# Performance work log

Hardware: AMD Instinct MI355X
Metric: run time of the kernel (lower is better)

Reference implementation:

```python
import jax, jax.numpy as jnp
import numpy as np

NOOBJ_LAMBDA = 0.5
COORD_LAMBDA = 5.0


def _cxcywh_to_xyxy(b):
    cx, cy, w, h = b[..., 0], b[..., 1], b[..., 2], b[..., 3]
    return jnp.stack([cx - w / 2, cy - h / 2, cx + w / 2, cy + h / 2], axis=-1)


def _pairwise_iou(a, b):
    # a: [B, N, 4] xyxy (preds), b: [B, M, 4] xyxy (targets) -> [B, N, M]
    lt = jnp.maximum(a[:, :, None, :2], b[:, None, :, :2])
    rb = jnp.minimum(a[:, :, None, 2:], b[:, None, :, 2:])
    wh = jnp.clip(rb - lt, 0.0)
    inter = wh[..., 0] * wh[..., 1]
    area_a = (a[..., 2] - a[..., 0]) * (a[..., 3] - a[..., 1])
    area_b = (b[..., 2] - b[..., 0]) * (b[..., 3] - b[..., 1])
    union = area_a[:, :, None] + area_b[:, None, :] - inter
    return inter / jnp.where(union > 0, union, 1.0)


def setup_inputs() -> dict:
    key = jax.random.key(0)
    kp, kt, km = jax.random.split(key, 3)
    B = 8192
    # positive values so sqrt(w), sqrt(h) is well-defined (as the torch code assumes)
    pred = jax.random.uniform(kp, (B, 7, 7, 30), dtype=jnp.float32, minval=0.05, maxval=1.0)
    target = jax.random.uniform(kt, (B, 7, 7, 30), dtype=jnp.float32, minval=0.05, maxval=1.0)
    # target confidence channel (index 4) is the obj/noobj indicator: 0 or 1
    obj = (jax.random.uniform(km, (B, 7, 7)) < 0.2).astype(jnp.float32)
    target = target.at[..., 4].set(obj)
    return {"pred_tensor": pred, "target_tensor": target}


def reference(pred_tensor, target_tensor):
    B = pred_tensor.shape[0]
    pred = pred_tensor.reshape(B, 49, 30)
    target = target_tensor.reshape(B, 49, 30)

    conf_t = target[..., 4]            # [B,49]
    noobj = conf_t == 0                # [B,49]
    obj = conf_t > 0                   # [B,49]

    # --- no-object confidence loss (channels 4 and 9) ---
    d4 = pred[..., 4] - target[..., 4]
    d9 = pred[..., 9] - target[..., 9]
    noobj_loss = jnp.sum(jnp.where(noobj, d4 * d4 + d9 * d9, 0.0))

    # --- object cells: 2 boxes per cell, padded to all 49 cells with a mask ---
    pb = pred[..., :10].reshape(B, 98, 5)
    tb = target[..., :10].reshape(B, 98, 5)
    box_mask = jnp.repeat(obj, 2, axis=1)  # [B,98]

    p_xyxy = _cxcywh_to_xyxy(pb[..., :4])
    t_xyxy = _cxcywh_to_xyxy(tb[..., :4])
    iou = _pairwise_iou(p_xyxy, t_xyxy)  # [B,98,98]
    pair_mask = box_mask[:, :, None] & box_mask[:, None, :]
    iou = jnp.where(pair_mask, iou, 0.0)
    max_iou = jnp.max(iou, axis=1)       # max over pred boxes, per target box [B,98]
    cmask = (max_iou != 0) & box_mask    # [B,98]

    cm = cmask.astype(pred.dtype)
    # coord (cx,cy) loss
    dxy = pb[..., :2] - tb[..., :2]
    coord_loss_cxcy = jnp.sum(cm * jnp.sum(dxy * dxy, axis=-1))
    # coord (sqrt w, sqrt h) loss
    dwh = jnp.sqrt(pb[..., 2:4]) - jnp.sqrt(tb[..., 2:4])
    coord_loss_wh = jnp.sum(cm * jnp.sum(dwh * dwh, axis=-1))
    # object confidence loss
    dconf = pb[..., 4] - tb[..., 4]
    obj_loss = jnp.sum(cm * dconf * dconf)

    # --- class loss over object cells ---
    dcls = pred[..., 10:] - target[..., 10:]
    cls_loss = jnp.sum(obj.astype(pred.dtype) * jnp.sum(dcls * dcls, axis=-1))

    bsz = jnp.asarray(B, pred.dtype)
    batch_cls_loss = cls_loss / bsz
    batch_obj_loss = (obj_loss + noobj_loss * NOOBJ_LAMBDA) / bsz
    batch_coord_loss = (coord_loss_cxcy + coord_loss_wh) * COORD_LAMBDA / bsz
    batch_loss = batch_cls_loss + batch_obj_loss + batch_coord_loss
    return (batch_loss, batch_cls_loss, batch_obj_loss, batch_coord_loss)
```

## Files before the change

### kernel.cpp

```cpp
#include <hip/hip_runtime.h>

#define CH 30
#define CELLS 49
#define ROWF 1470
#define WPB 4

__device__ __forceinline__ float waveReduce(float v) {
    #pragma unroll
    for (int o = 32; o > 0; o >>= 1) v += __shfl_xor(v, o, 64);
    return v;
}

__global__ __launch_bounds__(256) void yolo_main(const float* __restrict__ pred,
                                                 const float* __restrict__ targ,
                                                 float* __restrict__ ws, int B,
                                                 int NB) {
    const int w = threadIdx.x >> 6;
    const int lane = threadIdx.x & 63;
    const int r = blockIdx.x * WPB + w;

    __shared__ float4 boxS[WPB][2 * CELLS];
    __shared__ int clist[WPB][CELLS];
    __shared__ float sred[WPB][3];

    float cls = 0.f, objc = 0.f, coord = 0.f;

    if (r < B) {
        const float* P = pred + (size_t)r * ROWF;
        const float* T = targ + (size_t)r * ROWF;

        const int cl = lane < CELLS ? lane : CELLS - 1;
        const float t4 = T[cl * CH + 4];
        const float p4 = P[cl * CH + 4];
        const float t9 = T[cl * CH + 9];
        const float p9 = P[cl * CH + 9];

        const bool act = lane < CELLS;
        const bool isObj = act && (t4 > 0.f);
        const unsigned long long m = __ballot(isObj);

        if (act && !isObj) {
            const float d4 = p4 - t4, d9 = p9 - t9;
            objc += 0.5f * (d4 * d4 + d9 * d9);
        }

        const int nObj = __popcll(m);
        if (isObj) clist[w][__popcll(m & ((1ull << lane) - 1ull))] = lane;

        if (nObj) {
            const int nCls = nObj * 20;
            for (int base = 0; base < nCls; base += 64) {
                const int idx = base + lane;
                if (idx < nCls) {
                    const int cc = (idx * 3277) >> 16;
                    const int ch = 10 + (idx - cc * 20);
                    const int c = clist[w][cc];
                    const float dv = P[c * CH + ch] - T[c * CH + ch];
                    cls += dv * dv;
                }
            }

            const int nBox = 2 * nObj;
            for (int e = lane; e < nBox; e += 64) {
                const int c = clist[w][e >> 1];
                const float* pb = P + c * CH + (e & 1) * 5;
                const float cx = pb[0], cy = pb[1], bw = pb[2], bh = pb[3];
                boxS[w][e] = make_float4(cx - 0.5f * bw, cy - 0.5f * bh,
                                         cx + 0.5f * bw, cy + 0.5f * bh);
            }

            for (int e = lane; e < nBox; e += 64) {
                const int c = clist[w][e >> 1];
                const float* tb = T + c * CH + (e & 1) * 5;
                const float tcx = tb[0], tcy = tb[1], tw = tb[2], th = tb[3];
                const float tx1 = tcx - 0.5f * tw, ty1 = tcy - 0.5f * th;
                const float tx2 = tcx + 0.5f * tw, ty2 = tcy + 0.5f * th;
                const float ta = (tx2 - tx1) * (ty2 - ty1);
                float maxiou = 0.f;
                for (int i = 0; i < nBox; ++i) {
                    const float4 pb4 = boxS[w][i];
                    const float lx = fmaxf(pb4.x, tx1), ly = fmaxf(pb4.y, ty1);
                    const float rx = fminf(pb4.z, tx2), ry = fminf(pb4.w, ty2);
                    const float iw = fmaxf(rx - lx, 0.f), ih = fmaxf(ry - ly, 0.f);
                    const float inter = iw * ih;
                    const float pa = (pb4.z - pb4.x) * (pb4.w - pb4.y);
                    const float un = pa + ta - inter;
                    const float iou = inter / (un > 0.f ? un : 1.f);
                    maxiou = fmaxf(maxiou, iou);
                }
                if (maxiou != 0.f) {
                    const float* pb = P + c * CH + (e & 1) * 5;
                    const float dcx = pb[0] - tcx, dcy = pb[1] - tcy;
                    coord += dcx * dcx + dcy * dcy;
                    const float dw = sqrtf(pb[2]) - sqrtf(tw);
                    const float dh = sqrtf(pb[3]) - sqrtf(th);
                    coord += dw * dw + dh * dh;
                    const float dc = pb[4] - tb[4];
                    objc += dc * dc;
                }
            }
        }
    }

    cls = waveReduce(cls); objc = waveReduce(objc); coord = waveReduce(coord);
    if (lane == 0) { sred[w][0] = cls; sred[w][1] = objc; sred[w][2] = coord; }
    __syncthreads();
    if (threadIdx.x == 0) {
        float C = 0.f, O = 0.f, X = 0.f;
        #pragma unroll
        for (int k = 0; k < WPB; ++k) { C += sred[k][0]; O += sred[k][1]; X += sred[k][2]; }
        ws[blockIdx.x] = C;
        ws[NB + blockIdx.x] = O;
        ws[2 * NB + blockIdx.x] = X;
    }
}

__global__ __launch_bounds__(1024) void yolo_reduce(const float* __restrict__ ws,
                                                    float* __restrict__ out,
                                                    int NB, float invB) {
    const int tid = threadIdx.x;
    const int w = tid >> 6, lane = tid & 63;
    float c = 0.f, o = 0.f, x = 0.f;
    for (int i = tid; i < NB; i += 1024) {
        c += ws[i];
        o += ws[NB + i];
        x += ws[2 * NB + i];
    }
    c = waveReduce(c); o = waveReduce(o); x = waveReduce(x);
    __shared__ float sred[16][3];
    if (lane == 0) { sred[w][0] = c; sred[w][1] = o; sred[w][2] = x; }
    __syncthreads();
    if (tid == 0) {
        float C = 0.f, O = 0.f, X = 0.f;
        #pragma unroll
        for (int k = 0; k < 16; ++k) { C += sred[k][0]; O += sred[k][1]; X += sred[k][2]; }
        const float bcls = C * invB;
        const float bobj = O * invB;
        const float bcoord = X * 5.0f * invB;
        out[0] = bcls + bobj + bcoord;
        out[1] = bcls;
        out[2] = bobj;
        out[3] = bcoord;
    }
}

extern "C" void kernel_launch(void* const* d_in, const int* in_sizes, int n_in,
                              void* d_out, int out_size, void* d_ws, size_t ws_size,
                              hipStream_t stream) {
    const float* pred = (const float*)d_in[0];
    const float* targ = (const float*)d_in[1];
    float* ws = (float*)d_ws;
    float* out = (float*)d_out;
    const int B = in_sizes[0] / ROWF;
    const int NB = (B + WPB - 1) / WPB;

    yolo_main<<<NB, 256, 0, stream>>>(pred, targ, ws, B, NB);
    yolo_reduce<<<1, 1024, 0, stream>>>(ws, out, NB, 1.0f / (float)B);
}
```

Measured before the change: 126.2 us.

## Stage two rows per wave into LDS with direct global-to-LDS loads

Each wave now handles two consecutive batch rows and copies both pred and target rows in full into shared memory using global_load_lds 16-byte transfers, replacing scattered per-element global reads. Class and no-object losses are then computed from LDS in a dense, coalesced sweep over all channels, weighted by the object mask, while the IoU matching reads boxes from LDS. Blocks shrink to 128 threads, and each wave uses about 23KB of LDS, which may limit occupancy. The sweep also reads every class channel, including those of non-object cells.

```diff
diff --git a/kernel.cpp b/kernel.cpp
--- a/kernel.cpp
+++ b/kernel.cpp
@@ -3,7 +3,11 @@
 #define CH 30
 #define CELLS 49
 #define ROWF 1470
-#define WPB 4
+#define REGF 2940
+#define WPB 2
+#define RPBLK 4
+#define FULLI 11
+#define TAILL 31
 
 __device__ __forceinline__ float waveReduce(float v) {
     #pragma unroll
@@ -11,55 +15,148 @@
     return v;
 }
 
-__global__ __launch_bounds__(256) void yolo_main(const float* __restrict__ pred,
+__global__ __launch_bounds__(128) void yolo_main(const float* __restrict__ pred,
                                                  const float* __restrict__ targ,
                                                  float* __restrict__ ws, int B,
                                                  int NB) {
     const int w = threadIdx.x >> 6;
     const int lane = threadIdx.x & 63;
-    const int r = blockIdx.x * WPB + w;
-
+    const int r0 = (blockIdx.x * WPB + w) * 2;
+
+    __shared__ float stage[WPB][2][REGF];
     __shared__ float4 boxS[WPB][2 * CELLS];
     __shared__ int clist[WPB][CELLS];
     __shared__ float sred[WPB][3];
 
     float cls = 0.f, objc = 0.f, coord = 0.f;
 
-    if (r < B) {
-        const float* P = pred + (size_t)r * ROWF;
-        const float* T = targ + (size_t)r * ROWF;
-
-        const int cl = lane < CELLS ? lane : CELLS - 1;
-        const float t4 = T[cl * CH + 4];
-        const float p4 = P[cl * CH + 4];
-        const float t9 = T[cl * CH + 9];
-        const float p9 = P[cl * CH + 9];
-
+    if (r0 < B && (B - r0) >= 2) {
+        const float* P = pred + (size_t)r0 * ROWF;
+        const float* T = targ + (size_t)r0 * ROWF;
+        float* lP = &stage[w][0][0];
+        float* lT = &stage[w][1][0];
+
+        #pragma unroll
+        for (int k = 0; k < FULLI; ++k) {
+            __builtin_amdgcn_global_load_lds(
+                (const __attribute__((address_space(1))) float*)(P + k * 256 + lane * 4),
+                (__attribute__((address_space(3))) float*)(lP + k * 256), 16, 0, 0);
+            __builtin_amdgcn_global_load_lds(
+                (const __attribute__((address_space(1))) float*)(T + k * 256 + lane * 4),
+                (__attribute__((address_space(3))) float*)(lT + k * 256), 16, 0, 0);
+        }
+        if (lane < TAILL) {
+            __builtin_amdgcn_global_load_lds(
+                (const __attribute__((address_space(1))) float*)(P + FULLI * 256 + lane * 4),
+                (__attribute__((address_space(3))) float*)(lP + FULLI * 256), 16, 0, 0);
+            __builtin_amdgcn_global_load_lds(
+                (const __attribute__((address_space(1))) float*)(T + FULLI * 256 + lane * 4),
+                (__attribute__((address_space(3))) float*)(lT + FULLI * 256), 16, 0, 0);
+        }
+
+        asm volatile("s_waitcnt vmcnt(0)" ::: "memory");
+
+        const int cc = lane < CELLS ? lane : CELLS - 1;
+        unsigned long long m[2];
+        m[0] = __ballot((lane < CELLS) && (lT[cc * CH + 4] > 0.f));
+        m[1] = __ballot((lane < CELLS) && (lT[ROWF + cc * CH + 4] > 0.f));
+
+        #pragma unroll
+        for (int k = 0; k < 23; ++k) {
+            const int q = lane + k * 64;
+            if (q < 2 * 735) {
+                const int row = q >= 735;
+                const int pr = q - row * 735;
+                const int cell = (pr * 17477) >> 18;
+                const int ch0 = 2 * (pr - cell * 15);
+                const float wobj = (float)((m[row] >> cell) & 1ull);
+                const float2 pq = *(const float2*)(lP + 2 * q);
+                const float2 tq = *(const float2*)(lT + 2 * q);
+                const float dx = pq.x - tq.x, dy = pq.y - tq.y;
+                cls += (ch0 >= 10) ? wobj * (dx * dx + dy * dy) : 0.f;
+                const float nn = (ch0 == 4 ? dx * dx : 0.f)
+                               + (ch0 == 8 ? dy * dy : 0.f);
+                objc += 0.5f * (1.f - wobj) * nn;
+            }
+        }
+
+        for (int row = 0; row < 2; ++row) {
+            const unsigned long long mask = m[row];
+            const int nBox = 2 * __popcll(mask);
+            if (!nBox) continue;
+            const float* Pr = lP + row * ROWF;
+            const float* Tr = lT + row * ROWF;
+            const bool isObj = (lane < CELLS) && ((mask >> lane) & 1ull);
+            if (isObj) clist[w][__popcll(mask & ((1ull << lane) - 1ull))] = lane;
+
+            for (int e = lane; e < nBox; e += 64) {
+                const int c = clist[w][e >> 1];
+                const float* pb = Pr + c * CH + (e & 1) * 5;
+                const float cx = pb[0], cy = pb[1], bw = pb[2], bh = pb[3];
+                boxS[w][e] = make_float4(cx - 0.5f * bw, cy - 0.5f * bh,
+                                         cx + 0.5f * bw, cy + 0.5f * bh);
+            }
+
+            for (int e = lane; e < nBox; e += 64) {
+                const int c = clist[w][e >> 1];
+                const float* tb = Tr + c * CH + (e & 1) * 5;
+                const float tcx = tb[0], tcy = tb[1], tw = tb[2], th = tb[3];
+                const float tx1 = tcx - 0.5f * tw, ty1 = tcy - 0.5f * th;
+                const float tx2 = tcx + 0.5f * tw, ty2 = tcy + 0.5f * th;
+                const float ta = (tx2 - tx1) * (ty2 - ty1);
+                float maxiou = 0.f;
+                for (int i = 0; i < nBox; ++i) {
+                    const float4 pb4 = boxS[w][i];
+                    const float lx = fmaxf(pb4.x, tx1), ly = fmaxf(pb4.y, ty1);
+                    const float rx = fminf(pb4.z, tx2), ry = fminf(pb4.w, ty2);
+                    const float iw = fmaxf(rx - lx, 0.f), ih = fmaxf(ry - ly, 0.f);
+                    const float inter = iw * ih;
+                    const float pa = (pb4.z - pb4.x) * (pb4.w - pb4.y);
+                    const float un = pa + ta - inter;
+                    const float iou = inter / (un > 0.f ? un : 1.f);
+                    maxiou = fmaxf(maxiou, iou);
+                }
+                if (maxiou != 0.f) {
+                    const float* pb = Pr + c * CH + (e & 1) * 5;
+                    const float dcx = pb[0] - tcx, dcy = pb[1] - tcy;
+                    coord += dcx * dcx + dcy * dcy;
+                    const float dw = sqrtf(pb[2]) - sqrtf(tw);
+                    const float dh = sqrtf(pb[3]) - sqrtf(th);
+                    coord += dw * dw + dh * dh;
+                    const float dc = pb[4] - tb[4];
+                    objc += dc * dc;
+                }
+            }
+        }
+    } else if (r0 < B) {
+        const float* P = pred + (size_t)r0 * ROWF;
+        const float* T = targ + (size_t)r0 * ROWF;
+        const int cc = lane < CELLS ? lane : CELLS - 1;
+        const float t4 = T[cc * CH + 4];
+        const float p4 = P[cc * CH + 4];
+        const float t9 = T[cc * CH + 9];
+        const float p9 = P[cc * CH + 9];
         const bool act = lane < CELLS;
         const bool isObj = act && (t4 > 0.f);
-        const unsigned long long m = __ballot(isObj);
-
+        const unsigned long long mask = __ballot(isObj);
         if (act && !isObj) {
             const float d4 = p4 - t4, d9 = p9 - t9;
             objc += 0.5f * (d4 * d4 + d9 * d9);
         }
-
-        const int nObj = __popcll(m);
-        if (isObj) clist[w][__popcll(m & ((1ull << lane) - 1ull))] = lane;
-
+        const int nObj = __popcll(mask);
+        if (isObj) clist[w][__popcll(mask & ((1ull << lane) - 1ull))] = lane;
         if (nObj) {
             const int nCls = nObj * 20;
             for (int base = 0; base < nCls; base += 64) {
                 const int idx = base + lane;
                 if (idx < nCls) {
-                    const int cc = (idx * 3277) >> 16;
-                    const int ch = 10 + (idx - cc * 20);
-                    const int c = clist[w][cc];
+                    const int ccc = (idx * 3277) >> 16;
+                    const int ch = 10 + (idx - ccc * 20);
+                    const int c = clist[w][ccc];
                     const float dv = P[c * CH + ch] - T[c * CH + ch];
                     cls += dv * dv;
                 }
             }
-
             const int nBox = 2 * nObj;
             for (int e = lane; e < nBox; e += 64) {
                 const int c = clist[w][e >> 1];
@@ -68,7 +165,6 @@
                 boxS[w][e] = make_float4(cx - 0.5f * bw, cy - 0.5f * bh,
                                          cx + 0.5f * bw, cy + 0.5f * bh);
             }
-
             for (int e = lane; e < nBox; e += 64) {
                 const int c = clist[w][e >> 1];
                 const float* tb = T + c * CH + (e & 1) * 5;
@@ -152,8 +248,8 @@
     float* ws = (float*)d_ws;
     float* out = (float*)d_out;
     const int B = in_sizes[0] / ROWF;
-    const int NB = (B + WPB - 1) / WPB;
-
-    yolo_main<<<NB, 256, 0, stream>>>(pred, targ, ws, B, NB);
+    const int NB = (B + RPBLK - 1) / RPBLK;
+
+    yolo_main<<<NB, 128, 0, stream>>>(pred, targ, ws, B, NB);
     yolo_reduce<<<1, 1024, 0, stream>>>(ws, out, NB, 1.0f / (float)B);
 }
```

Result: slower. 132.7 us (+5.1%).

## Stream rows into LDS with double-buffered async global_load_lds in persistent waves

Applied to the files above, without the earlier changes.

Converts the kernel to a persistent grid (768 blocks of 2 waves), where each wave loops over rows and prefetches the next row's pred and target into LDS using async global-to-LDS loads, double-buffered and sequenced with explicit waitcnt. The class and no-object losses are now computed as a dense coalesced float2 sweep over the whole staged row with obj-mask weights, replacing scattered per-object gathers. The aim is to overlap memory latency with compute and keep the bandwidth-bound read fully coalesced. In exchange it relies on hand-tuned vmcnt counts and a fixed block count, and adds a large LDS footprint per block that may reduce occupancy.

```diff
diff --git a/kernel.cpp b/kernel.cpp
--- a/kernel.cpp
+++ b/kernel.cpp
@@ -3,7 +3,11 @@
 #define CH 30
 #define CELLS 49
 #define ROWF 1470
-#define WPB 4
+#define WPB 2
+#define NBLK 768
+#define FULLI 22
+#define TAILL 62
+#define BUFF 1472
 
 __device__ __forceinline__ float waveReduce(float v) {
     #pragma unroll
@@ -11,67 +15,97 @@
     return v;
 }
 
-__global__ __launch_bounds__(256) void yolo_main(const float* __restrict__ pred,
+__global__ __launch_bounds__(128) void yolo_main(const float* __restrict__ pred,
                                                  const float* __restrict__ targ,
                                                  float* __restrict__ ws, int B,
-                                                 int NB) {
+                                                 int NW) {
     const int w = threadIdx.x >> 6;
     const int lane = threadIdx.x & 63;
-    const int r = blockIdx.x * WPB + w;
+    const int wid = blockIdx.x * WPB + w;
 
+    __shared__ float stage[WPB][2][2][BUFF];
     __shared__ float4 boxS[WPB][2 * CELLS];
     __shared__ int clist[WPB][CELLS];
     __shared__ float sred[WPB][3];
 
     float cls = 0.f, objc = 0.f, coord = 0.f;
 
-    if (r < B) {
-        const float* P = pred + (size_t)r * ROWF;
-        const float* T = targ + (size_t)r * ROWF;
+    auto issueRow = [&](int row, int buf) {
+        const float* P = pred + (size_t)row * ROWF;
+        const float* T = targ + (size_t)row * ROWF;
+        float* lp = &stage[w][buf][0][0];
+        float* lt = &stage[w][buf][1][0];
+        #pragma unroll
+        for (int k = 0; k < FULLI; ++k) {
+            __builtin_amdgcn_global_load_lds(
+                (const __attribute__((address_space(1))) float*)(P + k * 64 + lane),
+                (__attribute__((address_space(3))) float*)(lp + k * 64), 4, 0, 0);
+            __builtin_amdgcn_global_load_lds(
+                (const __attribute__((address_space(1))) float*)(T + k * 64 + lane),
+                (__attribute__((address_space(3))) float*)(lt + k * 64), 4, 0, 0);
+        }
+        if (lane < TAILL) {
+            __builtin_amdgcn_global_load_lds(
+                (const __attribute__((address_space(1))) float*)(P + FULLI * 64 + lane),
+                (__attribute__((address_space(3))) float*)(lp + FULLI * 64), 4, 0, 0);
+            __builtin_amdgcn_global_load_lds(
+                (const __attribute__((address_space(1))) float*)(T + FULLI * 64 + lane),
+                (__attribute__((address_space(3))) float*)(lt + FULLI * 64), 4, 0, 0);
+        }
+    };
 
-        const int cl = lane < CELLS ? lane : CELLS - 1;
-        const float t4 = T[cl * CH + 4];
-        const float p4 = P[cl * CH + 4];
-        const float t9 = T[cl * CH + 9];
-        const float p9 = P[cl * CH + 9];
+    if (wid < B) issueRow(wid, 0);
 
-        const bool act = lane < CELLS;
-        const bool isObj = act && (t4 > 0.f);
-        const unsigned long long m = __ballot(isObj);
+    int it = 0;
+    for (int row = wid; row < B; row += NW, ++it) {
+        const int cur = it & 1;
+        const int nxt = row + NW;
 
-        if (act && !isObj) {
-            const float d4 = p4 - t4, d9 = p9 - t9;
-            objc += 0.5f * (d4 * d4 + d9 * d9);
+        asm volatile("s_waitcnt lgkmcnt(0)" ::: "memory");
+        if (nxt < B) {
+            issueRow(nxt, cur ^ 1);
+            asm volatile("s_waitcnt vmcnt(46)" ::: "memory");
+        } else {
+            asm volatile("s_waitcnt vmcnt(0)" ::: "memory");
         }
 
-        const int nObj = __popcll(m);
+        const float* lp = &stage[w][cur][0][0];
+        const float* lt = &stage[w][cur][1][0];
+
+        const int cc = lane < CELLS ? lane : CELLS - 1;
+        const bool isObj = (lane < CELLS) && (lt[cc * CH + 4] > 0.f);
+        const unsigned long long m = __ballot(isObj);
         if (isObj) clist[w][__popcll(m & ((1ull << lane) - 1ull))] = lane;
 
-        if (nObj) {
-            const int nCls = nObj * 20;
-            for (int base = 0; base < nCls; base += 64) {
-                const int idx = base + lane;
-                if (idx < nCls) {
-                    const int cc = (idx * 3277) >> 16;
-                    const int ch = 10 + (idx - cc * 20);
-                    const int c = clist[w][cc];
-                    const float dv = P[c * CH + ch] - T[c * CH + ch];
-                    cls += dv * dv;
-                }
+        #pragma unroll
+        for (int k = 0; k < 12; ++k) {
+            const int q = lane + k * 64;
+            if (q < 735) {
+                const int cell = (q * 17477) >> 18;
+                const int ch0 = 2 * (q - cell * 15);
+                const float wobj = (float)((m >> cell) & 1ull);
+                const float2 pq = *(const float2*)(lp + 2 * q);
+                const float2 tq = *(const float2*)(lt + 2 * q);
+                const float dx = pq.x - tq.x, dy = pq.y - tq.y;
+                cls += (ch0 >= 10) ? wobj * (dx * dx + dy * dy) : 0.f;
+                const float nn = (ch0 == 4 ? dx * dx : 0.f)
+                               + (ch0 == 8 ? dy * dy : 0.f);
+                objc += 0.5f * (1.f - wobj) * nn;
             }
+        }
 
-            const int nBox = 2 * nObj;
+        const int nBox = 2 * __popcll(m);
+        if (nBox) {
             for (int e = lane; e < nBox; e += 64) {
                 const int c = clist[w][e >> 1];
-                const float* pb = P + c * CH + (e & 1) * 5;
+                const float* pb = lp + c * CH + (e & 1) * 5;
                 const float cx = pb[0], cy = pb[1], bw = pb[2], bh = pb[3];
                 boxS[w][e] = make_float4(cx - 0.5f * bw, cy - 0.5f * bh,
                                          cx + 0.5f * bw, cy + 0.5f * bh);
             }
-
             for (int e = lane; e < nBox; e += 64) {
                 const int c = clist[w][e >> 1];
-                const float* tb = T + c * CH + (e & 1) * 5;
+                const float* tb = lt + c * CH + (e & 1) * 5;
                 const float tcx = tb[0], tcy = tb[1], tw = tb[2], th = tb[3];
                 const float tx1 = tcx - 0.5f * tw, ty1 = tcy - 0.5f * th;
                 const float tx2 = tcx + 0.5f * tw, ty2 = tcy + 0.5f * th;
@@ -89,7 +123,7 @@
                     maxiou = fmaxf(maxiou, iou);
                 }
                 if (maxiou != 0.f) {
-                    const float* pb = P + c * CH + (e & 1) * 5;
+                    const float* pb = lp + c * CH + (e & 1) * 5;
                     const float dcx = pb[0] - tcx, dcy = pb[1] - tcy;
                     coord += dcx * dcx + dcy * dcy;
                     const float dw = sqrtf(pb[2]) - sqrtf(tw);
@@ -110,8 +144,8 @@
         #pragma unroll
         for (int k = 0; k < WPB; ++k) { C += sred[k][0]; O += sred[k][1]; X += sred[k][2]; }
         ws[blockIdx.x] = C;
-        ws[NB + blockIdx.x] = O;
-        ws[2 * NB + blockIdx.x] = X;
+        ws[NBLK + blockIdx.x] = O;
+        ws[2 * NBLK + blockIdx.x] = X;
     }
 }
 
@@ -152,8 +186,8 @@
     float* ws = (float*)d_ws;
     float* out = (float*)d_out;
     const int B = in_sizes[0] / ROWF;
-    const int NB = (B + WPB - 1) / WPB;
+    const int NW = NBLK * WPB;
 
-    yolo_main<<<NB, 256, 0, stream>>>(pred, targ, ws, B, NB);
-    yolo_reduce<<<1, 1024, 0, stream>>>(ws, out, NB, 1.0f / (float)B);
+    yolo_main<<<NBLK, 128, 0, stream>>>(pred, targ, ws, B, NW);
+    yolo_reduce<<<1, 1024, 0, stream>>>(ws, out, NBLK, 1.0f / (float)B);
 }
```

New measurement: 129.7 us. +2.8%, slower.

## Stage full pred/target rows into LDS via direct global-to-LDS loads

Applied to the files above, without the earlier changes.

Each wave now copies its entire 1470-float pred and target rows into shared memory using coalesced global_load_lds instructions. Each lane then reads its own cell's 30 channels from LDS into registers, replacing the earlier scattered global gathers and the compacted cell-list indirection. Class loss and the IoU/coordinate work are computed per object cell by that cell's own lane. Blocks shrink to 2 waves because of the larger LDS footprint (about 24KB per block). That may limit occupancy, and lanes holding non-object cells sit idle during the per-cell work.

```diff
diff --git a/kernel.cpp b/kernel.cpp
--- a/kernel.cpp
+++ b/kernel.cpp
@@ -3,7 +3,9 @@
 #define CH 30
 #define CELLS 49
 #define ROWF 1470
-#define WPB 4
+#define WPB 2
+#define FULLI 22
+#define TAILL 62
 
 __device__ __forceinline__ float waveReduce(float v) {
     #pragma unroll
@@ -11,7 +13,7 @@
     return v;
 }
 
-__global__ __launch_bounds__(256) void yolo_main(const float* __restrict__ pred,
+__global__ __launch_bounds__(128) void yolo_main(const float* __restrict__ pred,
                                                  const float* __restrict__ targ,
                                                  float* __restrict__ ws, int B,
                                                  int NB) {
@@ -19,8 +21,8 @@
     const int lane = threadIdx.x & 63;
     const int r = blockIdx.x * WPB + w;
 
+    __shared__ float stage[WPB][2][ROWF];
     __shared__ float4 boxS[WPB][2 * CELLS];
-    __shared__ int clist[WPB][CELLS];
     __shared__ float sred[WPB][3];
 
     float cls = 0.f, objc = 0.f, coord = 0.f;
@@ -28,51 +30,78 @@
     if (r < B) {
         const float* P = pred + (size_t)r * ROWF;
         const float* T = targ + (size_t)r * ROWF;
+        float* lP = &stage[w][0][0];
+        float* lT = &stage[w][1][0];
 
-        const int cl = lane < CELLS ? lane : CELLS - 1;
-        const float t4 = T[cl * CH + 4];
-        const float p4 = P[cl * CH + 4];
-        const float t9 = T[cl * CH + 9];
-        const float p9 = P[cl * CH + 9];
+        #pragma unroll
+        for (int k = 0; k < FULLI; ++k) {
+            __builtin_amdgcn_global_load_lds(
+                (const __attribute__((address_space(1))) float*)(P + k * 64 + lane),
+                (__attribute__((address_space(3))) float*)(lP + k * 64), 4, 0, 0);
+            __builtin_amdgcn_global_load_lds(
+                (const __attribute__((address_space(1))) float*)(T + k * 64 + lane),
+                (__attribute__((address_space(3))) float*)(lT + k * 64), 4, 0, 0);
+        }
+        if (lane < TAILL) {
+            __builtin_amdgcn_global_load_lds(
+                (const __attribute__((address_space(1))) float*)(P + FULLI * 64 + lane),
+                (__attribute__((address_space(3))) float*)(lP + FULLI * 64), 4, 0, 0);
+            __builtin_amdgcn_global_load_lds(
+                (const __attribute__((address_space(1))) float*)(T + FULLI * 64 + lane),
+                (__attribute__((address_space(3))) float*)(lT + FULLI * 64), 4, 0, 0);
+        }
+        asm volatile("s_waitcnt vmcnt(0)" ::: "memory");
 
         const bool act = lane < CELLS;
-        const bool isObj = act && (t4 > 0.f);
+        const int c = act ? lane : CELLS - 1;
+        const float2* pc = (const float2*)(lP + c * CH);
+        const float2* tc = (const float2*)(lT + c * CH);
+
+        float2 pA[15], tA[15];
+        #pragma unroll
+        for (int j = 0; j < 15; ++j) { pA[j] = pc[j]; tA[j] = tc[j]; }
+
+        const bool isObj = act && (tA[2].x > 0.f);
         const unsigned long long m = __ballot(isObj);
+        const int nBox = 2 * __popcll(m);
 
         if (act && !isObj) {
-            const float d4 = p4 - t4, d9 = p9 - t9;
+            const float d4 = pA[2].x - tA[2].x;
+            const float d9 = pA[4].y - tA[4].y;
             objc += 0.5f * (d4 * d4 + d9 * d9);
         }
 
-        const int nObj = __popcll(m);
-        if (isObj) clist[w][__popcll(m & ((1ull << lane) - 1ull))] = lane;
+        if (isObj) {
+            #pragma unroll
+            for (int j = 5; j < 15; ++j) {
+                const float dx = pA[j].x - tA[j].x;
+                const float dy = pA[j].y - tA[j].y;
+                cls += dx * dx + dy * dy;
+            }
+            const int rank = __popcll(m & ((1ull << lane) - 1ull));
+            boxS[w][2 * rank] = make_float4(pA[0].x - 0.5f * pA[1].x,
+                                            pA[0].y - 0.5f * pA[1].y,
+                                            pA[0].x + 0.5f * pA[1].x,
+                                            pA[0].y + 0.5f * pA[1].y);
+            boxS[w][2 * rank + 1] = make_float4(pA[2].y - 0.5f * pA[3].y,
+                                                pA[3].x - 0.5f * pA[4].x,
+                                                pA[2].y + 0.5f * pA[3].y,
+                                                pA[3].x + 0.5f * pA[4].x);
+        }
 
-        if (nObj) {
-            const int nCls = nObj * 20;
-            for (int base = 0; base < nCls; base += 64) {
-                const int idx = base + lane;
-                if (idx < nCls) {
-                    const int cc = (idx * 3277) >> 16;
-                    const int ch = 10 + (idx - cc * 20);
-                    const int c = clist[w][cc];
-                    const float dv = P[c * CH + ch] - T[c * CH + ch];
-                    cls += dv * dv;
-                }
-            }
-
-            const int nBox = 2 * nObj;
-            for (int e = lane; e < nBox; e += 64) {
-                const int c = clist[w][e >> 1];
-                const float* pb = P + c * CH + (e & 1) * 5;
-                const float cx = pb[0], cy = pb[1], bw = pb[2], bh = pb[3];
-                boxS[w][e] = make_float4(cx - 0.5f * bw, cy - 0.5f * bh,
-                                         cx + 0.5f * bw, cy + 0.5f * bh);
-            }
-
-            for (int e = lane; e < nBox; e += 64) {
-                const int c = clist[w][e >> 1];
-                const float* tb = T + c * CH + (e & 1) * 5;
-                const float tcx = tb[0], tcy = tb[1], tw = tb[2], th = tb[3];
+        if (isObj) {
+            #pragma unroll
+            for (int s = 0; s < 2; ++s) {
+                const float tcx = s ? tA[2].y : tA[0].x;
+                const float tcy = s ? tA[3].x : tA[0].y;
+                const float tw  = s ? tA[3].y : tA[1].x;
+                const float th  = s ? tA[4].x : tA[1].y;
+                const float pcx = s ? pA[2].y : pA[0].x;
+                const float pcy = s ? pA[3].x : pA[0].y;
+                const float pw  = s ? pA[3].y : pA[1].x;
+                const float ph  = s ? pA[4].x : pA[1].y;
+                const float pcf = s ? pA[4].y : pA[2].x;
+                const float tcf = s ? tA[4].y : tA[2].x;
                 const float tx1 = tcx - 0.5f * tw, ty1 = tcy - 0.5f * th;
                 const float tx2 = tcx + 0.5f * tw, ty2 = tcy + 0.5f * th;
                 const float ta = (tx2 - tx1) * (ty2 - ty1);
@@ -89,13 +118,12 @@
                     maxiou = fmaxf(maxiou, iou);
                 }
                 if (maxiou != 0.f) {
-                    const float* pb = P + c * CH + (e & 1) * 5;
-                    const float dcx = pb[0] - tcx, dcy = pb[1] - tcy;
+                    const float dcx = pcx - tcx, dcy = pcy - tcy;
                     coord += dcx * dcx + dcy * dcy;
-                    const float dw = sqrtf(pb[2]) - sqrtf(tw);
-                    const float dh = sqrtf(pb[3]) - sqrtf(th);
+                    const float dw = sqrtf(pw) - sqrtf(tw);
+                    const float dh = sqrtf(ph) - sqrtf(th);
                     coord += dw * dw + dh * dh;
-                    const float dc = pb[4] - tb[4];
+                    const float dc = pcf - tcf;
                     objc += dc * dc;
                 }
             }
@@ -154,6 +182,6 @@
     const int B = in_sizes[0] / ROWF;
     const int NB = (B + WPB - 1) / WPB;
 
-    yolo_main<<<NB, 256, 0, stream>>>(pred, targ, ws, B, NB);
+    yolo_main<<<NB, 128, 0, stream>>>(pred, targ, ws, B, NB);
     yolo_reduce<<<1, 1024, 0, stream>>>(ws, out, NB, 1.0f / (float)B);
 }
```

Result: slower. 133.8 us (+6.0%).
